# Kernel tuning notes

Hardware: AMD Instinct MI355X
Metric: run time of the kernel (lower is better)

Reference implementation:

```python
import jax, jax.numpy as jnp
import numpy as np
from jax import lax

NUM_HEADS = 4
FIN = 4096
FOUT = 4096


def setup_inputs() -> dict:
    key = jax.random.key(0)
    k1, k2, k3, k4, k5 = jax.random.split(key, 5)
    inp = jax.random.normal(k1, (2, 2048, FIN), dtype=jnp.float32)
    # xavier-uniform-like scale for the fc weight
    lim = float(np.sqrt(6.0 / (FIN + FOUT)))
    W = jax.random.uniform(k2, (FOUT, FIN), minval=-lim, maxval=lim, dtype=jnp.float32)
    # per-head 3x3 conv kernels (Conv2d(1, 1, 3, 3) per head, stacked OIHW)
    conv_w = jax.random.normal(k3, (NUM_HEADS, 1, 3, 3), dtype=jnp.float32) * (1.0 / 3.0)
    conv_b = jax.random.normal(k4, (NUM_HEADS,), dtype=jnp.float32) * 0.1
    sk_wt = jax.random.normal(k5, (NUM_HEADS, 1, 1), dtype=jnp.float32)
    return {"inp": inp, "W": W, "conv_w": conv_w, "conv_b": conv_b, "sk_wt": sk_wt}


def _transform_weight(W, conv_w, conv_b, sk_wt):
    # W: [fout, fin] -> [num_heads, fout/num_heads, fin]
    mat = W.reshape(NUM_HEADS, FOUT // NUM_HEADS, FIN)
    # per-head 3x3 conv == grouped conv with feature_group_count = num_heads
    x = mat[None]  # [1, H=num_heads, fout/h, fin]
    y = lax.conv_general_dilated(
        x, conv_w,
        window_strides=(1, 1),
        padding=((1, 1), (1, 1)),
        feature_group_count=NUM_HEADS,
        dimension_numbers=("NCHW", "OIHW", "NCHW"),
    )[0] + conv_b[:, None, None]
    # sigmoid-gated residual: out + sigmoid(sk_wt) * mat
    out = y + jax.nn.sigmoid(sk_wt) * mat
    return out.reshape(FOUT, FIN)


def reference(inp, W, conv_w, conv_b, sk_wt):
    W_i = _transform_weight(W, conv_w, conv_b, sk_wt)
    # F.linear(inp, W_i) with bias=None
    return jnp.einsum("bsf,of->bso", inp, W_i)
```

## Files before the change

kernel.cpp:

```cpp
#include <hip/hip_runtime.h>
#include <hip/hip_bf16.h>

#define FIN 4096
#define FOUT 4096
#define HEADS 4
#define ROWS_PER_HEAD (FOUT / HEADS)
#define M_DIM 4096

typedef __attribute__((ext_vector_type(8))) short bf16x8;
typedef __attribute__((ext_vector_type(4))) float floatx4;

#define CAST_BLOCKS ((M_DIM * FIN) / (256 * 8))
#define TRANS_BLOCKS ((FOUT * FIN / 8) / 256)

__global__ __launch_bounds__(256) void prep(
    const float* __restrict__ x,
    __hip_bfloat16* __restrict__ y,
    const float* __restrict__ W,
    const float* __restrict__ cw,
    const float* __restrict__ cb,
    const float* __restrict__ sk,
    __hip_bfloat16* __restrict__ Wt) {
  if (blockIdx.x < CAST_BLOCKS) {
    int idx = blockIdx.x * 256 + threadIdx.x;
    const float4* xv = (const float4*)x;
    float4 a = xv[idx * 2];
    float4 b = xv[idx * 2 + 1];
    __hip_bfloat16 t[8];
    t[0] = __float2bfloat16(a.x); t[1] = __float2bfloat16(a.y);
    t[2] = __float2bfloat16(a.z); t[3] = __float2bfloat16(a.w);
    t[4] = __float2bfloat16(b.x); t[5] = __float2bfloat16(b.y);
    t[6] = __float2bfloat16(b.z); t[7] = __float2bfloat16(b.w);
    *(bf16x8*)(&y[(size_t)idx * 8]) = *(bf16x8*)t;
    return;
  }

  int gid = (blockIdx.x - CAST_BLOCKS) * 256 + threadIdx.x;
  int o = gid >> 9;
  int fs = (gid & 511) << 3;
  int h = o >> 10;
  int r = o & (ROWS_PER_HEAD - 1);

  float kk[3][3];
#pragma unroll
  for (int i = 0; i < 3; i++)
#pragma unroll
    for (int j = 0; j < 3; j++) kk[i][j] = cw[h * 9 + i * 3 + j];
  float sig = 1.0f / (1.0f + __expf(-sk[h]));

  float acc[8];
#pragma unroll
  for (int j = 0; j < 8; j++) acc[j] = cb[h];

#pragma unroll
  for (int dr = -1; dr <= 1; dr++) {
    int rr = r + dr;
    if (rr < 0 || rr >= ROWS_PER_HEAD) continue;
    const float* rp = W + ((size_t)(h * ROWS_PER_HEAD + rr)) * FIN + fs;
    float a[10];
    float4 v0 = *(const float4*)rp;
    float4 v1 = *(const float4*)(rp + 4);
    a[1] = v0.x; a[2] = v0.y; a[3] = v0.z; a[4] = v0.w;
    a[5] = v1.x; a[6] = v1.y; a[7] = v1.z; a[8] = v1.w;
    a[0] = (fs > 0) ? rp[-1] : 0.0f;
    a[9] = (fs + 8 < FIN) ? rp[8] : 0.0f;
#pragma unroll
    for (int j = 0; j < 8; j++)
      acc[j] += kk[dr + 1][0] * a[j] + kk[dr + 1][1] * a[j + 1] +
                kk[dr + 1][2] * a[j + 2];
    if (dr == 0) {
#pragma unroll
      for (int j = 0; j < 8; j++) acc[j] += sig * a[j + 1];
    }
  }
  __hip_bfloat16 t[8];
#pragma unroll
  for (int j = 0; j < 8; j++) t[j] = __float2bfloat16(acc[j]);
  *(bf16x8*)(&Wt[(size_t)o * FIN + fs]) = *(bf16x8*)t;
}

__device__ static inline void gload_lds16(const void* g, void* l) {
  __builtin_amdgcn_global_load_lds(
      (const __attribute__((address_space(1))) void*)g,
      (__attribute__((address_space(3))) void*)l, 16, 0, 0);
}

__global__ __launch_bounds__(256, 3) void gemm_nt(
    const __hip_bfloat16* __restrict__ A,
    const __hip_bfloat16* __restrict__ B,
    float* __restrict__ C,
    int M, int N, int K) {
  __shared__ __hip_bfloat16 As[128 * 64];
  __shared__ __hip_bfloat16 Bs[128 * 64];

  const int tid = threadIdx.x;
  const int lane = tid & 63;
  const int wave = tid >> 6;
  const int tile_m = blockIdx.y * 128;
  const int tile_n = blockIdx.x * 128;

  const int fr = lane & 15;
  const int quad = lane >> 4;
  const int wm = (wave & 1) * 64;
  const int wn = (wave >> 1) * 64;
  const int selA = fr & 7;

  floatx4 acc[4][4];
#pragma unroll
  for (int i = 0; i < 4; i++)
#pragma unroll
    for (int j = 0; j < 4; j++) acc[i][j] = (floatx4){0.f, 0.f, 0.f, 0.f};

  for (int k0 = 0; k0 < K; k0 += 64) {
#pragma unroll
    for (int t = 0; t < 4; t++) {
      int base = (t * 4 + wave) * 64;
      int p = base + lane;
      int row = p >> 3;
      int g = (p & 7) ^ (row & 7);
      gload_lds16(&A[(size_t)(tile_m + row) * K + k0 + g * 8],
                  &As[base * 8]);
      gload_lds16(&B[(size_t)(tile_n + row) * K + k0 + g * 8],
                  &Bs[base * 8]);
    }
    __syncthreads();

#pragma unroll
    for (int kk = 0; kk < 2; kk++) {
      const int sA = ((kk * 4 + quad) ^ selA) * 8;
      bf16x8 a_frag[4], b_frag[4];
#pragma unroll
      for (int i = 0; i < 4; i++) {
        a_frag[i] = *(const bf16x8*)(&As[(wm + i * 16 + fr) * 64 + sA]);
        b_frag[i] = *(const bf16x8*)(&Bs[(wn + i * 16 + fr) * 64 + sA]);
      }
#pragma unroll
      for (int i = 0; i < 4; i++)
#pragma unroll
        for (int j = 0; j < 4; j++)
          acc[i][j] = __builtin_amdgcn_mfma_f32_16x16x32_bf16(
              a_frag[i], b_frag[j], acc[i][j], 0, 0, 0);
    }
    __syncthreads();
  }

#pragma unroll
  for (int i = 0; i < 4; i++) {
    int m_base = tile_m + wm + i * 16 + quad * 4;
#pragma unroll
    for (int j = 0; j < 4; j++) {
      int n = tile_n + wn + j * 16 + fr;
#pragma unroll
      for (int r = 0; r < 4; r++) {
        C[(size_t)(m_base + r) * N + n] = acc[i][j][r];
      }
    }
  }
}

extern "C" void kernel_launch(void* const* d_in, const int* in_sizes, int n_in,
                              void* d_out, int out_size, void* d_ws,
                              size_t ws_size, hipStream_t stream) {
  const float* inp = (const float*)d_in[0];
  const float* W = (const float*)d_in[1];
  const float* conv_w = (const float*)d_in[2];
  const float* conv_b = (const float*)d_in[3];
  const float* sk_wt = (const float*)d_in[4];
  float* out = (float*)d_out;

  __hip_bfloat16* Wt = (__hip_bfloat16*)d_ws;
  __hip_bfloat16* Ab =
      (__hip_bfloat16*)((char*)d_ws + (size_t)(32u << 20));

  prep<<<CAST_BLOCKS + TRANS_BLOCKS, 256, 0, stream>>>(inp, Ab, W, conv_w,
                                                       conv_b, sk_wt, Wt);
  dim3 grid(FOUT / 128, M_DIM / 128);
  gemm_nt<<<grid, 256, 0, stream>>>(Ab, Wt, out, M_DIM, FOUT, FIN);
}
```

Measured before the change: 293.5 us.

## Rewrite bf16 GEMM as 256x256 tile, 8-wave, double-buffered pipelined kernel

Replaces the 128x128 single-buffered GEMM with a 256x256 tile on 512 threads. The kernel double-buffers LDS in half-tiles and interleaves global-to-LDS loads for upcoming k-tiles with the MFMA phases, using raised wave priority during the matrix ops. This is meant to hide global memory latency and improve operand reuse per block. In exchange it uses more LDS and registers, lowers occupancy, and launches only 256 blocks on a 256-CU device.

```diff
diff --git a/kernel.cpp b/kernel.cpp
--- a/kernel.cpp
+++ b/kernel.cpp
@@ -85,74 +85,197 @@
       (__attribute__((address_space(3))) void*)l, 16, 0, 0);
 }
 
-__global__ __launch_bounds__(256, 3) void gemm_nt(
+#define BK 64
+#define NT (FIN / BK)
+
+__global__ __launch_bounds__(512, 2) void gemm_nt(
     const __hip_bfloat16* __restrict__ A,
     const __hip_bfloat16* __restrict__ B,
     float* __restrict__ C,
     int M, int N, int K) {
-  __shared__ __hip_bfloat16 As[128 * 64];
-  __shared__ __hip_bfloat16 Bs[128 * 64];
+  __shared__ __hip_bfloat16 As[2][2][128 * BK];
+  __shared__ __hip_bfloat16 Bs[2][2][128 * BK];
 
   const int tid = threadIdx.x;
   const int lane = tid & 63;
   const int wave = tid >> 6;
-  const int tile_m = blockIdx.y * 128;
-  const int tile_n = blockIdx.x * 128;
-
+  const int wr = wave >> 2;
+  const int wn = wave & 3;
   const int fr = lane & 15;
   const int quad = lane >> 4;
-  const int wm = (wave & 1) * 64;
-  const int wn = (wave >> 1) * 64;
-  const int selA = fr & 7;
-
-  floatx4 acc[4][4];
-#pragma unroll
-  for (int i = 0; i < 4; i++)
+  const int sel = fr & 7;
+  const int tile_m = blockIdx.y * 256;
+  const int tile_n = blockIdx.x * 256;
+
+  const __hip_bfloat16* At = A + (size_t)tile_m * K;
+  const __hip_bfloat16* Bt = B + (size_t)tile_n * K;
+
+  int soff[2], doff[2];
+#pragma unroll
+  for (int c = 0; c < 2; c++) {
+    int p = c * 512 + tid;
+    int row = p >> 3;
+    int g = (p & 7) ^ (row & 7);
+    soff[c] = row * K + g * 8;
+    doff[c] = p * 8;
+  }
+  int aro[4], bro[2], co[2];
+#pragma unroll
+  for (int u = 0; u < 4; u++) aro[u] = (wr * 16 + u * 32 + fr) * 64;
+#pragma unroll
+  for (int j = 0; j < 2; j++) bro[j] = (wn * 16 + j * 64 + fr) * 64;
+#pragma unroll
+  for (int kk = 0; kk < 2; kk++) co[kk] = ((kk * 4 + quad) ^ sel) * 8;
+
+  floatx4 acc[8][4];
+#pragma unroll
+  for (int i = 0; i < 8; i++)
 #pragma unroll
     for (int j = 0; j < 4; j++) acc[i][j] = (floatx4){0.f, 0.f, 0.f, 0.f};
 
-  for (int k0 = 0; k0 < K; k0 += 64) {
-#pragma unroll
-    for (int t = 0; t < 4; t++) {
-      int base = (t * 4 + wave) * 64;
-      int p = base + lane;
-      int row = p >> 3;
-      int g = (p & 7) ^ (row & 7);
-      gload_lds16(&A[(size_t)(tile_m + row) * K + k0 + g * 8],
-                  &As[base * 8]);
-      gload_lds16(&B[(size_t)(tile_n + row) * K + k0 + g * 8],
-                  &Bs[base * 8]);
-    }
-    __syncthreads();
-
-#pragma unroll
-    for (int kk = 0; kk < 2; kk++) {
-      const int sA = ((kk * 4 + quad) ^ selA) * 8;
-      bf16x8 a_frag[4], b_frag[4];
-#pragma unroll
-      for (int i = 0; i < 4; i++) {
-        a_frag[i] = *(const bf16x8*)(&As[(wm + i * 16 + fr) * 64 + sA]);
-        b_frag[i] = *(const bf16x8*)(&Bs[(wn + i * 16 + fr) * 64 + sA]);
-      }
-#pragma unroll
-      for (int i = 0; i < 4; i++)
-#pragma unroll
-        for (int j = 0; j < 4; j++)
-          acc[i][j] = __builtin_amdgcn_mfma_f32_16x16x32_bf16(
-              a_frag[i], b_frag[j], acc[i][j], 0, 0, 0);
-    }
-    __syncthreads();
-  }
-
-#pragma unroll
-  for (int i = 0; i < 4; i++) {
-    int m_base = tile_m + wm + i * 16 + quad * 4;
+  bf16x8 af[4][2];
+  bf16x8 bf[2][2][2];
+
+#define STAGE(GBASE, LARR, TILE, BUF, HALF)                              \
+  do {                                                                   \
+    const __hip_bfloat16* _s =                                           \
+        GBASE + (size_t)(HALF) * 128 * K + (size_t)(TILE) * BK;          \
+    __hip_bfloat16* _d = &LARR[BUF][HALF][0];                            \
+    _Pragma("unroll") for (int _c = 0; _c < 2; _c++) {                   \
+      gload_lds16(_s + soff[_c], _d + doff[_c]);                         \
+    }                                                                    \
+  } while (0)
+
+#define LOADA(BUF, MH)                                                   \
+  do {                                                                   \
+    const __hip_bfloat16* _b = &As[BUF][MH][0];                          \
+    _Pragma("unroll") for (int _u = 0; _u < 4; _u++) {                   \
+      _Pragma("unroll") for (int _kk = 0; _kk < 2; _kk++) {              \
+        af[_u][_kk] = *(const bf16x8*)&_b[aro[_u] + co[_kk]];            \
+      }                                                                  \
+    }                                                                    \
+  } while (0)
+
+#define LOADB(BUF, NH)                                                   \
+  do {                                                                   \
+    const __hip_bfloat16* _b = &Bs[BUF][NH][0];                          \
+    _Pragma("unroll") for (int _j = 0; _j < 2; _j++) {                   \
+      _Pragma("unroll") for (int _kk = 0; _kk < 2; _kk++) {              \
+        bf[NH][_j][_kk] = *(const bf16x8*)&_b[bro[_j] + co[_kk]];        \
+      }                                                                  \
+    }                                                                    \
+  } while (0)
+
+#define MMA(MH, NH)                                                      \
+  do {                                                                   \
+    __builtin_amdgcn_s_setprio(1);                                       \
+    _Pragma("unroll") for (int _kk = 0; _kk < 2; _kk++) {                \
+      _Pragma("unroll") for (int _u = 0; _u < 4; _u++) {                 \
+        _Pragma("unroll") for (int _j = 0; _j < 2; _j++) {               \
+          acc[(MH) * 4 + _u][(NH) * 2 + _j] =                            \
+              __builtin_amdgcn_mfma_f32_16x16x32_bf16(                   \
+                  af[_u][_kk], bf[NH][_j][_kk],                          \
+                  acc[(MH) * 4 + _u][(NH) * 2 + _j], 0, 0, 0);           \
+        }                                                                \
+      }                                                                  \
+    }                                                                    \
+    __builtin_amdgcn_s_setprio(0);                                       \
+  } while (0)
+
+#define BAR() __builtin_amdgcn_s_barrier()
+#define WAITVM(N) asm volatile("s_waitcnt vmcnt(" #N ")" ::: "memory")
+
+  STAGE(At, As, 0, 0, 0);
+  STAGE(Bt, Bs, 0, 0, 1);
+  STAGE(At, As, 0, 0, 1);
+  STAGE(Bt, Bs, 0, 0, 0);
+  STAGE(At, As, 1, 1, 0);
+  STAGE(Bt, Bs, 1, 1, 1);
+  WAITVM(4);
+  BAR();
+
+#pragma unroll 2
+  for (int t = 0; t < NT - 2; ++t) {
+    const int buf = t & 1;
+    const int nbuf = buf ^ 1;
+    LOADA(buf, 0);
+    LOADB(buf, 0);
+    STAGE(At, As, t + 1, nbuf, 1);
+    BAR();
+    MMA(0, 0);
+    BAR();
+    LOADB(buf, 1);
+    STAGE(Bt, Bs, t + 1, nbuf, 0);
+    BAR();
+    MMA(0, 1);
+    BAR();
+    LOADA(buf, 1);
+    STAGE(At, As, t + 2, buf, 0);
+    BAR();
+    MMA(1, 1);
+    BAR();
+    STAGE(Bt, Bs, t + 2, buf, 1);
+    BAR();
+    MMA(1, 0);
+    WAITVM(4);
+    BAR();
+  }
+
+  {
+    LOADA(0, 0);
+    LOADB(0, 0);
+    STAGE(At, As, NT - 1, 1, 1);
+    BAR();
+    MMA(0, 0);
+    BAR();
+    LOADB(0, 1);
+    STAGE(Bt, Bs, NT - 1, 1, 0);
+    BAR();
+    MMA(0, 1);
+    BAR();
+    LOADA(0, 1);
+    BAR();
+    MMA(1, 1);
+    BAR();
+    BAR();
+    MMA(1, 0);
+    WAITVM(0);
+    BAR();
+  }
+  {
+    LOADA(1, 0);
+    LOADB(1, 0);
+    BAR();
+    MMA(0, 0);
+    BAR();
+    LOADB(1, 1);
+    BAR();
+    MMA(0, 1);
+    BAR();
+    LOADA(1, 1);
+    BAR();
+    MMA(1, 1);
+    BAR();
+    BAR();
+    MMA(1, 0);
+  }
+
+#undef STAGE
+#undef LOADA
+#undef LOADB
+#undef MMA
+#undef BAR
+#undef WAITVM
+
+#pragma unroll
+  for (int i = 0; i < 8; i++) {
+    int mb = tile_m + wr * 16 + i * 32 + quad * 4;
 #pragma unroll
     for (int j = 0; j < 4; j++) {
-      int n = tile_n + wn + j * 16 + fr;
+      int n = tile_n + wn * 16 + j * 64 + fr;
 #pragma unroll
       for (int r = 0; r < 4; r++) {
-        C[(size_t)(m_base + r) * N + n] = acc[i][j][r];
+        C[(size_t)(mb + r) * N + n] = acc[i][j][r];
       }
     }
   }
@@ -174,6 +297,6 @@
 
   prep<<<CAST_BLOCKS + TRANS_BLOCKS, 256, 0, stream>>>(inp, Ab, W, conv_w,
                                                        conv_b, sk_wt, Wt);
-  dim3 grid(FOUT / 128, M_DIM / 128);
-  gemm_nt<<<grid, 256, 0, stream>>>(Ab, Wt, out, M_DIM, FOUT, FIN);
+  dim3 grid(FOUT / 256, M_DIM / 256);
+  gemm_nt<<<grid, 512, 0, stream>>>(Ab, Wt, out, M_DIM, FOUT, FIN);
 }
```

Measured after the change: 302.6 us. 1.03x slower.
